# Kernel tuning notes

Hardware: AMD Instinct MI355X
Metric: run time of the kernel (lower is better)

The kernel has to match this reference:

```python
import jax, jax.numpy as jnp
from jax import lax
import numpy as np

N, W, H, C = 32, 64, 64, 256
D_STYLE = 256


def setup_inputs() -> dict:
    key = jax.random.key(0)
    k1, k2, k3, k4 = jax.random.split(key, 4)
    inputs = jax.random.normal(k1, (N, W, H, C), dtype=jnp.float32)
    style_coding = jax.random.normal(k2, (N, D_STYLE), dtype=jnp.float32)
    # he_normal-ish init scaling for the learned weights
    w_dense = jax.random.normal(k3, (D_STYLE, C), dtype=jnp.float32) * np.sqrt(2.0 / D_STYLE)
    w_conv = jax.random.normal(k4, (1, 1, C, C), dtype=jnp.float32) * np.sqrt(2.0 / C)
    return {"inputs": inputs, "style_coding": style_coding, "w_dense": w_dense, "w_conv": w_conv}


def reference(inputs, style_coding, w_dense, w_conv):
    # inputs: [N,W,H,C] (NHWC), style_coding: [N,D_style]
    c = inputs.shape[-1]
    scale = 1.0 / jnp.sqrt(jnp.float32(c))
    # Dense(fout_dim, use_bias=False, activation=LeakyReLU())  (keras default alpha=0.3)
    q = jax.nn.leaky_relu(style_coding @ w_dense, negative_slope=0.3)  # [N,C]
    # channel-wise attention: einsum('nwhc,nwhc->nc') with q broadcast over w,h
    ca_logits = jnp.einsum('nwhc,nc->nc', inputs, q) * scale           # [N,C]
    ca = jax.nn.softmax(ca_logits, axis=-1)[:, None, None, :]          # [N,1,1,C]
    # position-wise attention: einsum('nwhc,nwhc->nwh'), softmax over flattened W*H
    pa_logits = jnp.einsum('nwhc,nc->nwh', inputs, q) * scale          # [N,W,H]
    n, w, h = pa_logits.shape
    pa = jax.nn.softmax(pa_logits.reshape(n, w * h), axis=1).reshape(n, w, h, 1)
    x = inputs * ca * pa                                               # [N,W,H,C]
    # DarknetConv2D_BN_Leaky with no norm kwarg: 1x1 conv (no bias) + LeakyReLU(0.1)
    y = lax.conv_general_dilated(x, w_conv, window_strides=(1, 1), padding='SAME',
                                 dimension_numbers=('NHWC', 'HWIO', 'NHWC'))
    return jax.nn.leaky_relu(y, negative_slope=0.1)
```

## Files before the change

### kernel.cpp

```cpp
#include <hip/hip_runtime.h>
#include <hip/hip_bf16.h>


#define NBATCH 32
#define PIX 4096
#define CH 256
#define SCALE 0.0625f

typedef __attribute__((ext_vector_type(8))) short short8;
typedef __attribute__((ext_vector_type(4))) short short4v;
typedef __attribute__((ext_vector_type(4))) float floatx4;

__device__ __forceinline__ short f2bf(float x) {
    unsigned u = __builtin_bit_cast(unsigned, x);
    u += 0x7fffu + ((u >> 16) & 1u);
    return (short)(u >> 16);
}

__global__ __launch_bounds__(256) void style_kernel(
    const float* __restrict__ style, const float* __restrict__ wd,
    float* __restrict__ q, float* __restrict__ colsum)
{
    __shared__ float s[256];
    const int n = blockIdx.x, t = threadIdx.x;
    s[t] = style[n * 256 + t];
    __syncthreads();
    float acc = 0.f;
#pragma unroll 8
    for (int k = 0; k < 256; ++k) acc += s[k] * wd[k * 256 + t];
    q[n * 256 + t] = acc > 0.f ? acc : 0.3f * acc;
    colsum[n * 256 + t] = 0.f;
}

__global__ void wt_kernel(const float* __restrict__ wc, short* __restrict__ wT)
{
    __shared__ float tile[32][33];
    const int co0 = blockIdx.x * 32, ci0 = blockIdx.y * 32;
    const int tx = threadIdx.x, ty = threadIdx.y;
#pragma unroll
    for (int r = 0; r < 4; ++r)
        tile[ty + r * 8][tx] = wc[(ci0 + ty + r * 8) * 256 + co0 + tx];
    __syncthreads();
#pragma unroll
    for (int r = 0; r < 4; ++r)
        wT[(co0 + ty + r * 8) * 256 + ci0 + tx] = f2bf(tile[tx][ty + r * 8]);
}

__global__ __launch_bounds__(256) void reduce_kernel(
    const float* __restrict__ inp, const float* __restrict__ q,
    float* __restrict__ colsum, float* __restrict__ pa_logits)
{
    const int n = blockIdx.y;
    const int chunk = blockIdx.x;
    const int lane = threadIdx.x & 63, w = threadIdx.x >> 6;
    const float4 qv = *(const float4*)&q[n * 256 + lane * 4];
    float4 cs = make_float4(0.f, 0.f, 0.f, 0.f);
    const int pbase = chunk * 128 + w * 32;
    const float* base = inp + ((size_t)n * PIX + pbase) * CH;
    for (int j = 0; j < 32; ++j) {
        float4 v = *(const float4*)&base[(size_t)j * CH + lane * 4];
        float d = v.x * qv.x + v.y * qv.y + v.z * qv.z + v.w * qv.w;
        cs.x += v.x; cs.y += v.y; cs.z += v.z; cs.w += v.w;
#pragma unroll
        for (int off = 32; off; off >>= 1) d += __shfl_xor(d, off);
        if (lane == 0) pa_logits[n * PIX + pbase + j] = d * SCALE;
    }
    float* cp = colsum + n * 256 + lane * 4;
    atomicAdd(cp + 0, cs.x);
    atomicAdd(cp + 1, cs.y);
    atomicAdd(cp + 2, cs.z);
    atomicAdd(cp + 3, cs.w);
}

__global__ __launch_bounds__(256) void softmax_kernel(
    const float* __restrict__ colsum, const float* __restrict__ q,
    const float* __restrict__ pa_logits,
    float* __restrict__ ca, float* __restrict__ pa)
{
    __shared__ float red[256];
    const int n = blockIdx.x, t = threadIdx.x;

    float lg = colsum[n * 256 + t] * q[n * 256 + t] * SCALE;
    red[t] = lg; __syncthreads();
    for (int s = 128; s > 0; s >>= 1) {
        if (t < s) red[t] = fmaxf(red[t], red[t + s]);
        __syncthreads();
    }
    float m = red[0]; __syncthreads();
    float e = expf(lg - m);
    red[t] = e; __syncthreads();
    for (int s = 128; s > 0; s >>= 1) {
        if (t < s) red[t] += red[t + s];
        __syncthreads();
    }
    ca[n * 256 + t] = e / red[0];
    __syncthreads();

    float lv[16];
    float lmax = -1e30f;
#pragma unroll
    for (int i = 0; i < 16; ++i) {
        lv[i] = pa_logits[n * PIX + t + 256 * i];
        lmax = fmaxf(lmax, lv[i]);
    }
    red[t] = lmax; __syncthreads();
    for (int s = 128; s > 0; s >>= 1) {
        if (t < s) red[t] = fmaxf(red[t], red[t + s]);
        __syncthreads();
    }
    float M = red[0]; __syncthreads();
    float ev[16], lsum = 0.f;
#pragma unroll
    for (int i = 0; i < 16; ++i) { ev[i] = expf(lv[i] - M); lsum += ev[i]; }
    red[t] = lsum; __syncthreads();
    for (int s = 128; s > 0; s >>= 1) {
        if (t < s) red[t] += red[t + s];
        __syncthreads();
    }
    float inv = 1.0f / red[0];
#pragma unroll
    for (int i = 0; i < 16; ++i) pa[n * PIX + t + 256 * i] = ev[i] * inv;
}

__global__ __launch_bounds__(256) void conv_mfma(
    const float* __restrict__ inp, const float* __restrict__ ca,
    const float* __restrict__ pa, const short* __restrict__ wT,
    float* __restrict__ out)
{
    __shared__ __attribute__((aligned(16))) short As[128][72];
    __shared__ __attribute__((aligned(16))) short Bs[128][72];

    const int n   = blockIdx.z;
    const int m0  = blockIdx.y * 128;
    const int co0 = blockIdx.x * 128;
    const int tid = threadIdx.x;
    const int lane = tid & 63, wid = tid >> 6;
    const int wm = wid & 1, wn = wid >> 1;
    const int l16 = lane & 15, quad = lane >> 4;

    floatx4 acc[4][4] = {};

    const float* Abase = inp + ((size_t)(n * PIX + m0)) * CH;
    const short* Bbase = wT + (size_t)co0 * CH;

    const int akq = tid & 15, arb = tid >> 4;
    const int bck = tid & 7,  brb = tid >> 3;

    for (int kb = 0; kb < 4; ++kb) {
        const int k0 = kb * 64;
        if (kb) __syncthreads();
        const float4 cav = *(const float4*)&ca[n * 256 + k0 + akq * 4];
#pragma unroll
        for (int i = 0; i < 8; ++i) {
            const int r = arb + 16 * i;
            float4 v = *(const float4*)&Abase[(size_t)r * CH + k0 + akq * 4];
            short4v s;
            s.x = f2bf(v.x * cav.x);
            s.y = f2bf(v.y * cav.y);
            s.z = f2bf(v.z * cav.z);
            s.w = f2bf(v.w * cav.w);
            *(short4v*)&As[r][akq * 4] = s;
        }
#pragma unroll
        for (int i = 0; i < 4; ++i) {
            const int r = brb + 32 * i;
            *(uint4*)&Bs[r][bck * 8] = *(const uint4*)&Bbase[(size_t)r * CH + k0 + bck * 8];
        }
        __syncthreads();
#pragma unroll
        for (int kk = 0; kk < 64; kk += 32) {
            short8 af[4], bfr[4];
#pragma unroll
            for (int mt = 0; mt < 4; ++mt)
                af[mt] = *(const short8*)&As[wm * 64 + mt * 16 + l16][kk + quad * 8];
#pragma unroll
            for (int nt = 0; nt < 4; ++nt)
                bfr[nt] = *(const short8*)&Bs[wn * 64 + nt * 16 + l16][kk + quad * 8];
#pragma unroll
            for (int mt = 0; mt < 4; ++mt)
#pragma unroll
                for (int nt = 0; nt < 4; ++nt)
                    acc[mt][nt] = __builtin_amdgcn_mfma_f32_16x16x32_bf16(
                        af[mt], bfr[nt], acc[mt][nt], 0, 0, 0);
        }
    }

#pragma unroll
    for (int mt = 0; mt < 4; ++mt) {
#pragma unroll
        for (int reg = 0; reg < 4; ++reg) {
            const int pix = m0 + wm * 64 + mt * 16 + quad * 4 + reg;
            const float pav = pa[n * PIX + pix];
            float* orow = out + ((size_t)(n * PIX + pix)) * CH + co0 + wn * 64;
#pragma unroll
            for (int nt = 0; nt < 4; ++nt) {
                float z = acc[mt][nt][reg] * pav;
                orow[nt * 16 + l16] = z > 0.f ? z : 0.1f * z;
            }
        }
    }
}

extern "C" void kernel_launch(void* const* d_in, const int* in_sizes, int n_in,
                              void* d_out, int out_size, void* d_ws, size_t ws_size,
                              hipStream_t stream) {
    const float* inputs = (const float*)d_in[0];
    const float* style  = (const float*)d_in[1];
    const float* wdense = (const float*)d_in[2];
    const float* wconv  = (const float*)d_in[3];
    float* out = (float*)d_out;

    char* ws = (char*)d_ws;
    float* q         = (float*)(ws + 0);
    float* colsum    = (float*)(ws + 32768);
    float* ca        = (float*)(ws + 65536);
    float* pa_logits = (float*)(ws + 98304);
    float* pa        = (float*)(ws + 622592);
    short* wT        = (short*)(ws + 1146880);

    style_kernel<<<NBATCH, 256, 0, stream>>>(style, wdense, q, colsum);
    wt_kernel<<<dim3(8, 8), dim3(32, 8), 0, stream>>>(wconv, wT);
    reduce_kernel<<<dim3(32, NBATCH), 256, 0, stream>>>(inputs, q, colsum, pa_logits);
    softmax_kernel<<<NBATCH, 256, 0, stream>>>(colsum, q, pa_logits, ca, pa);
    conv_mfma<<<dim3(2, 32, NBATCH), 256, 0, stream>>>(inputs, ca, pa, wT, out);
}
```

Baseline: 314.5 us.

## Pre-cast inputs to bf16, fold channel attention into per-batch weights, use LDS DMA

The reduction pass now also writes a bf16 copy of the inputs. It stores per-block partial column sums instead of using atomics. The channel attention vector is folded into a per-batch scaled bf16 conv weight. The conv kernel computes all 256 output channels per 64-pixel tile, loading XOR-swizzled tiles straight into LDS with global_load_lds. This avoids re-reading and re-converting the fp32 input for each output-channel tile, at the cost of extra workspace and a bf16 round trip.

```diff
diff --git a/kernel.cpp b/kernel.cpp
--- a/kernel.cpp
+++ b/kernel.cpp
@@ -1,5 +1,4 @@
 #include <hip/hip_runtime.h>
-#include <hip/hip_bf16.h>
 
 
 #define NBATCH 32
@@ -17,9 +16,15 @@
     return (short)(u >> 16);
 }
 
+__device__ __forceinline__ void gll16(const void* g, void* l) {
+    __builtin_amdgcn_global_load_lds(
+        (const __attribute__((address_space(1))) unsigned int*)g,
+        (__attribute__((address_space(3))) unsigned int*)l, 16, 0, 0);
+}
+
 __global__ __launch_bounds__(256) void style_kernel(
     const float* __restrict__ style, const float* __restrict__ wd,
-    float* __restrict__ q, float* __restrict__ colsum)
+    float* __restrict__ q)
 {
     __shared__ float s[256];
     const int n = blockIdx.x, t = threadIdx.x;
@@ -29,26 +34,12 @@
 #pragma unroll 8
     for (int k = 0; k < 256; ++k) acc += s[k] * wd[k * 256 + t];
     q[n * 256 + t] = acc > 0.f ? acc : 0.3f * acc;
-    colsum[n * 256 + t] = 0.f;
-}
-
-__global__ void wt_kernel(const float* __restrict__ wc, short* __restrict__ wT)
-{
-    __shared__ float tile[32][33];
-    const int co0 = blockIdx.x * 32, ci0 = blockIdx.y * 32;
-    const int tx = threadIdx.x, ty = threadIdx.y;
-#pragma unroll
-    for (int r = 0; r < 4; ++r)
-        tile[ty + r * 8][tx] = wc[(ci0 + ty + r * 8) * 256 + co0 + tx];
-    __syncthreads();
-#pragma unroll
-    for (int r = 0; r < 4; ++r)
-        wT[(co0 + ty + r * 8) * 256 + ci0 + tx] = f2bf(tile[tx][ty + r * 8]);
-}
-
-__global__ __launch_bounds__(256) void reduce_kernel(
+}
+
+__global__ __launch_bounds__(256) void reduce_cast_kernel(
     const float* __restrict__ inp, const float* __restrict__ q,
-    float* __restrict__ colsum, float* __restrict__ pa_logits)
+    float* __restrict__ colsum_part, float* __restrict__ pa_logits,
+    short* __restrict__ bf16in)
 {
     const int n = blockIdx.y;
     const int chunk = blockIdx.x;
@@ -57,30 +48,33 @@
     float4 cs = make_float4(0.f, 0.f, 0.f, 0.f);
     const int pbase = chunk * 128 + w * 32;
     const float* base = inp + ((size_t)n * PIX + pbase) * CH;
+    short* obase = bf16in + ((size_t)n * PIX + pbase) * CH;
     for (int j = 0; j < 32; ++j) {
         float4 v = *(const float4*)&base[(size_t)j * CH + lane * 4];
         float d = v.x * qv.x + v.y * qv.y + v.z * qv.z + v.w * qv.w;
         cs.x += v.x; cs.y += v.y; cs.z += v.z; cs.w += v.w;
+        short4v sv;
+        sv.x = f2bf(v.x); sv.y = f2bf(v.y); sv.z = f2bf(v.z); sv.w = f2bf(v.w);
+        *(short4v*)&obase[(size_t)j * CH + lane * 4] = sv;
 #pragma unroll
         for (int off = 32; off; off >>= 1) d += __shfl_xor(d, off);
         if (lane == 0) pa_logits[n * PIX + pbase + j] = d * SCALE;
     }
-    float* cp = colsum + n * 256 + lane * 4;
-    atomicAdd(cp + 0, cs.x);
-    atomicAdd(cp + 1, cs.y);
-    atomicAdd(cp + 2, cs.z);
-    atomicAdd(cp + 3, cs.w);
+    *(float4*)&colsum_part[((size_t)n * 128 + chunk * 4 + w) * 256 + lane * 4] = cs;
 }
 
 __global__ __launch_bounds__(256) void softmax_kernel(
-    const float* __restrict__ colsum, const float* __restrict__ q,
+    const float* __restrict__ colsum_part, const float* __restrict__ q,
     const float* __restrict__ pa_logits,
     float* __restrict__ ca, float* __restrict__ pa)
 {
     __shared__ float red[256];
     const int n = blockIdx.x, t = threadIdx.x;
 
-    float lg = colsum[n * 256 + t] * q[n * 256 + t] * SCALE;
+    float csum = 0.f;
+#pragma unroll 8
+    for (int i = 0; i < 128; ++i) csum += colsum_part[((size_t)n * 128 + i) * 256 + t];
+    float lg = csum * q[n * 256 + t] * SCALE;
     red[t] = lg; __syncthreads();
     for (int s = 128; s > 0; s >>= 1) {
         if (t < s) red[t] = fmaxf(red[t], red[t + s]);
@@ -122,60 +116,70 @@
     for (int i = 0; i < 16; ++i) pa[n * PIX + t + 256 * i] = ev[i] * inv;
 }
 
-__global__ __launch_bounds__(256) void conv_mfma(
-    const float* __restrict__ inp, const float* __restrict__ ca,
-    const float* __restrict__ pa, const short* __restrict__ wT,
-    float* __restrict__ out)
-{
-    __shared__ __attribute__((aligned(16))) short As[128][72];
-    __shared__ __attribute__((aligned(16))) short Bs[128][72];
-
-    const int n   = blockIdx.z;
-    const int m0  = blockIdx.y * 128;
-    const int co0 = blockIdx.x * 128;
+__global__ void wscale_kernel(const float* __restrict__ wc,
+                              const float* __restrict__ ca,
+                              short* __restrict__ wscaled)
+{
+    __shared__ float tile[32][33];
+    const int n = blockIdx.z;
+    const int co0 = blockIdx.x * 32, ci0 = blockIdx.y * 32;
+    const int tx = threadIdx.x, ty = threadIdx.y;
+#pragma unroll
+    for (int r = 0; r < 4; ++r)
+        tile[ty + r * 8][tx] = wc[(ci0 + ty + r * 8) * 256 + co0 + tx];
+    const float cav = ca[n * 256 + ci0 + tx];
+    __syncthreads();
+#pragma unroll
+    for (int r = 0; r < 4; ++r)
+        wscaled[(size_t)n * 65536 + (co0 + ty + r * 8) * 256 + ci0 + tx] =
+            f2bf(tile[tx][ty + r * 8] * cav);
+}
+
+__global__ __launch_bounds__(256, 4) void conv_mfma(
+    const short* __restrict__ bf16in, const short* __restrict__ wscaled,
+    const float* __restrict__ pa, float* __restrict__ out)
+{
+    __shared__ __attribute__((aligned(16))) short As[64 * 64];
+    __shared__ __attribute__((aligned(16))) short Bs[256 * 64];
+
+    const int n  = blockIdx.y;
+    const int m0 = blockIdx.x * 64;
     const int tid = threadIdx.x;
     const int lane = tid & 63, wid = tid >> 6;
-    const int wm = wid & 1, wn = wid >> 1;
     const int l16 = lane & 15, quad = lane >> 4;
+    const int l8r = lane >> 3, slot = lane & 7;
 
     floatx4 acc[4][4] = {};
 
-    const float* Abase = inp + ((size_t)(n * PIX + m0)) * CH;
-    const short* Bbase = wT + (size_t)co0 * CH;
-
-    const int akq = tid & 15, arb = tid >> 4;
-    const int bck = tid & 7,  brb = tid >> 3;
+    const short* Agb = bf16in + ((size_t)n * PIX + m0) * CH;
+    const short* Bgb = wscaled + (size_t)n * 65536;
 
     for (int kb = 0; kb < 4; ++kb) {
         const int k0 = kb * 64;
         if (kb) __syncthreads();
-        const float4 cav = *(const float4*)&ca[n * 256 + k0 + akq * 4];
+#pragma unroll
+        for (int i = 0; i < 2; ++i) {
+            const int r = wid * 16 + i * 8 + l8r;
+            gll16(Agb + (size_t)r * CH + k0 + ((slot ^ (r & 7)) << 3),
+                  &As[(wid * 16 + i * 8) * 64]);
+        }
 #pragma unroll
         for (int i = 0; i < 8; ++i) {
-            const int r = arb + 16 * i;
-            float4 v = *(const float4*)&Abase[(size_t)r * CH + k0 + akq * 4];
-            short4v s;
-            s.x = f2bf(v.x * cav.x);
-            s.y = f2bf(v.y * cav.y);
-            s.z = f2bf(v.z * cav.z);
-            s.w = f2bf(v.w * cav.w);
-            *(short4v*)&As[r][akq * 4] = s;
-        }
-#pragma unroll
-        for (int i = 0; i < 4; ++i) {
-            const int r = brb + 32 * i;
-            *(uint4*)&Bs[r][bck * 8] = *(const uint4*)&Bbase[(size_t)r * CH + k0 + bck * 8];
-        }
-        __syncthreads();
-#pragma unroll
-        for (int kk = 0; kk < 64; kk += 32) {
+            const int c = wid * 64 + i * 8 + l8r;
+            gll16(Bgb + (size_t)c * CH + k0 + ((slot ^ (c & 7)) << 3),
+                  &Bs[(wid * 64 + i * 8) * 64]);
+        }
+        __syncthreads();
+#pragma unroll
+        for (int kk2 = 0; kk2 < 2; ++kk2) {
+            const int sx = ((kk2 * 4 + quad) ^ (l16 & 7)) << 3;
             short8 af[4], bfr[4];
 #pragma unroll
             for (int mt = 0; mt < 4; ++mt)
-                af[mt] = *(const short8*)&As[wm * 64 + mt * 16 + l16][kk + quad * 8];
+                af[mt] = *(const short8*)&As[(mt * 16 + l16) * 64 + sx];
 #pragma unroll
             for (int nt = 0; nt < 4; ++nt)
-                bfr[nt] = *(const short8*)&Bs[wn * 64 + nt * 16 + l16][kk + quad * 8];
+                bfr[nt] = *(const short8*)&Bs[(wid * 64 + nt * 16 + l16) * 64 + sx];
 #pragma unroll
             for (int mt = 0; mt < 4; ++mt)
 #pragma unroll
@@ -189,9 +193,9 @@
     for (int mt = 0; mt < 4; ++mt) {
 #pragma unroll
         for (int reg = 0; reg < 4; ++reg) {
-            const int pix = m0 + wm * 64 + mt * 16 + quad * 4 + reg;
+            const int pix = m0 + mt * 16 + quad * 4 + reg;
             const float pav = pa[n * PIX + pix];
-            float* orow = out + ((size_t)(n * PIX + pix)) * CH + co0 + wn * 64;
+            float* orow = out + ((size_t)(n * PIX + pix)) * CH + wid * 64;
 #pragma unroll
             for (int nt = 0; nt < 4; ++nt) {
                 float z = acc[mt][nt][reg] * pav;
@@ -211,16 +215,18 @@
     float* out = (float*)d_out;
 
     char* ws = (char*)d_ws;
-    float* q         = (float*)(ws + 0);
-    float* colsum    = (float*)(ws + 32768);
-    float* ca        = (float*)(ws + 65536);
-    float* pa_logits = (float*)(ws + 98304);
-    float* pa        = (float*)(ws + 622592);
-    short* wT        = (short*)(ws + 1146880);
-
-    style_kernel<<<NBATCH, 256, 0, stream>>>(style, wdense, q, colsum);
-    wt_kernel<<<dim3(8, 8), dim3(32, 8), 0, stream>>>(wconv, wT);
-    reduce_kernel<<<dim3(32, NBATCH), 256, 0, stream>>>(inputs, q, colsum, pa_logits);
-    softmax_kernel<<<NBATCH, 256, 0, stream>>>(colsum, q, pa_logits, ca, pa);
-    conv_mfma<<<dim3(2, 32, NBATCH), 256, 0, stream>>>(inputs, ca, pa, wT, out);
-}
+    float* q           = (float*)(ws + 0);
+    float* ca          = (float*)(ws + 32768);
+    float* pa_logits   = (float*)(ws + 65536);
+    float* pa          = (float*)(ws + 589824);
+    float* colsum_part = (float*)(ws + 1114112);
+    short* wscaled     = (short*)(ws + 5308416);
+    short* bf16in      = (short*)(ws + 9502720);
+
+    style_kernel<<<NBATCH, 256, 0, stream>>>(style, wdense, q);
+    reduce_cast_kernel<<<dim3(32, NBATCH), 256, 0, stream>>>(inputs, q, colsum_part,
+                                                             pa_logits, bf16in);
+    softmax_kernel<<<NBATCH, 256, 0, stream>>>(colsum_part, q, pa_logits, ca, pa);
+    wscale_kernel<<<dim3(8, 8, NBATCH), dim3(32, 8), 0, stream>>>(wconv, ca, wscaled);
+    conv_mfma<<<dim3(64, NBATCH), 256, 0, stream>>>(bf16in, wscaled, pa, out);
+}
```

Measured after the change: 316.5 us. No clear change (+0.7%).
